# Optimization experiments

Measured on AMD Instinct MI355X. Metric: run time of the kernel, lower is better.

Reference implementation:

```python
import jax, jax.numpy as jnp
import numpy as np

G = 4        # split_group
H = 64       # hidden_size_t = 256 // 4 (causal -> //1)
I = 64       # input_size_t  = 256 // 4
EPS = 1e-5


def _lstm(x, W_ih, W_hh, b):
    """Grouped unidirectional LSTM, PyTorch gate order (i,f,g,o).
    x: (G,B,T,I); W_ih: (G,4H,I); W_hh: (G,4H,H); b: (G,4H) -> (G,B,T,H)"""
    g, bsz, t, _ = x.shape
    h_dim = W_hh.shape[-1]
    # precompute input projections for all timesteps
    xp = jnp.einsum('gbti,gki->gbtk', x, W_ih) + b[:, None, None, :]  # (G,B,T,4H)
    xp = jnp.moveaxis(xp, 2, 0)  # (T,G,B,4H)

    def step(carry, xt):
        h, c = carry
        gates = xt + jnp.einsum('gbh,gkh->gbk', h, W_hh)
        i_g, f_g, g_g, o_g = jnp.split(gates, 4, axis=-1)
        i_g = jax.nn.sigmoid(i_g)
        f_g = jax.nn.sigmoid(f_g)
        g_g = jnp.tanh(g_g)
        o_g = jax.nn.sigmoid(o_g)
        c = f_g * c + i_g * g_g
        h = o_g * jnp.tanh(c)
        return (h, c), h

    h0 = jnp.zeros((g, bsz, h_dim), x.dtype)
    _, hs = jax.lax.scan(step, (h0, h0), xp)  # hs: (T,G,B,H)
    return jnp.moveaxis(hs, 0, 2)  # (G,B,T,H)


def _bn(x, gamma, beta):
    """BatchNorm1d (training stats) over (B,T) per feature. x: (B,T,F)"""
    mean = x.mean(axis=(0, 1))
    var = x.var(axis=(0, 1))
    return (x - mean) * jax.lax.rsqrt(var + EPS) * gamma + beta


def setup_inputs() -> dict:
    key = jax.random.key(0)
    ks = jax.random.split(key, 12)
    s = 0.1
    F = G * H
    return {
        'inpt': jax.random.normal(ks[0], (32, 1000, 256), jnp.float32),
        'W_ih1': jax.random.normal(ks[1], (G, 4 * H, I), jnp.float32) * s,
        'W_hh1': jax.random.normal(ks[2], (G, 4 * H, H), jnp.float32) * s,
        'b1': jax.random.normal(ks[3], (G, 4 * H), jnp.float32) * s,
        'W_ih2': jax.random.normal(ks[4], (G, 4 * H, H), jnp.float32) * s,
        'W_hh2': jax.random.normal(ks[5], (G, 4 * H, H), jnp.float32) * s,
        'b2': jax.random.normal(ks[6], (G, 4 * H), jnp.float32) * s,
        'gamma1': jnp.ones((F,), jnp.float32) + jax.random.normal(ks[7], (F,)) * 0.01,
        'beta1': jax.random.normal(ks[8], (F,), jnp.float32) * 0.01,
        'gamma2': jnp.ones((F,), jnp.float32) + jax.random.normal(ks[9], (F,)) * 0.01,
        'beta2': jax.random.normal(ks[10], (F,), jnp.float32) * 0.01,
    }


def reference(inpt, W_ih1, W_hh1, b1, W_ih2, W_hh2, b2, gamma1, beta1, gamma2, beta2):
    B, T, F = inpt.shape
    # chunk along features -> (G,B,T,I)
    xg = jnp.transpose(inpt.reshape(B, T, G, I), (2, 0, 1, 3))
    y1 = _lstm(xg, W_ih1, W_hh1, b1)  # (G,B,T,H)
    # torch.stack(dim=-1) + flatten: feature index = h*G + g (interleaved)
    x = jnp.transpose(y1, (1, 2, 3, 0)).reshape(B, T, H * G)
    x = _bn(x, gamma1, beta1)
    # chunk again into G contiguous groups of size H
    xg2 = jnp.transpose(x.reshape(B, T, G, H), (2, 0, 1, 3))
    y2 = _lstm(xg2, W_ih2, W_hh2, b2)  # (G,B,T,H)
    # torch.cat(dim=-1): contiguous groups
    x = jnp.transpose(y2, (1, 2, 0, 3)).reshape(B, T, G * H)
    x = _bn(x, gamma2, beta2)
    return x
```

## Files before the change

kernel.cpp:

```cpp
#include <hip/hip_runtime.h>
#include <math.h>

#define G 4
#define H 64
#define T 1000
#define B 32
#define F 256
#define ROWS (B*T)

__device__ __forceinline__ float sigm(float x) {
    return 1.f / (1.f + __expf(-x));
}
__device__ __forceinline__ float tanh_f(float x) {
    return 2.f / (1.f + __expf(-2.f * x)) - 1.f;
}

template<int LAYER>
__global__ __launch_bounds__(256, 1)
void rec_kernel(const float* __restrict__ xin,
                const float* __restrict__ Wih,
                const float* __restrict__ Whh,
                const float* __restrict__ bias,
                const float* __restrict__ bnac,
                float* __restrict__ out)
{
    const int g = blockIdx.x & 3;
    const int b = blockIdx.x >> 2;
    const int k = threadIdx.x;

    __shared__ __align__(16) float xsh[2][64];
    __shared__ __align__(16) float hsh[64];
    __shared__ __align__(16) float gsh[256];

    float wih[64], whh[64];
    {
        const float4* wi = (const float4*)(Wih + (size_t)(g * 256 + k) * 64);
        const float4* wh = (const float4*)(Whh + (size_t)(g * 256 + k) * 64);
        #pragma unroll
        for (int i = 0; i < 16; ++i) {
            float4 v = wi[i];
            wih[4*i] = v.x; wih[4*i+1] = v.y; wih[4*i+2] = v.z; wih[4*i+3] = v.w;
            float4 u = wh[i];
            whh[4*i] = u.x; whh[4*i+1] = u.y; whh[4*i+2] = u.z; whh[4*i+3] = u.w;
        }
    }
    const float bk = bias[g * 256 + k];

    const long rowbase = (long)b * T;
    const int  colbase = g * 64;

    float c = 0.f, af = 1.f, cf = 0.f;
    float xa = 0.f, xb = 0.f;

    if (k < 64) {
        if (LAYER == 2) { af = bnac[colbase + k]; cf = bnac[256 + colbase + k]; }
        hsh[k] = 0.f;
        float x0 = xin[(rowbase + 0) * 256 + colbase + k];
        xsh[0][k] = (LAYER == 2) ? fmaf(x0, af, cf) : x0;
        int t1 = (1 < T) ? 1 : T - 1;
        int t2 = (2 < T) ? 2 : T - 1;
        xa = xin[(rowbase + t1) * 256 + colbase + k];
        xb = xin[(rowbase + t2) * 256 + colbase + k];
    }
    __syncthreads();

    for (int t = 0; t < T; ++t) {
        const int cur = t & 1;

        float xn = 0.f;
        if (k < 64) {
            int tp = t + 3; if (tp > T - 1) tp = T - 1;
            xn = xin[(rowbase + tp) * 256 + colbase + k];
        }

        const float* xs = xsh[cur];
        float a0 = 0.f, a1 = 0.f, a2 = 0.f, a3 = 0.f;
        #pragma unroll
        for (int i = 0; i < 64; i += 4) {
            a0 = fmaf(wih[i],     xs[i],     a0);
            a1 = fmaf(wih[i + 1], xs[i + 1], a1);
            a2 = fmaf(wih[i + 2], xs[i + 2], a2);
            a3 = fmaf(wih[i + 3], xs[i + 3], a3);
        }
        #pragma unroll
        for (int j = 0; j < 64; j += 4) {
            a0 = fmaf(whh[j],     hsh[j],     a0);
            a1 = fmaf(whh[j + 1], hsh[j + 1], a1);
            a2 = fmaf(whh[j + 2], hsh[j + 2], a2);
            a3 = fmaf(whh[j + 3], hsh[j + 3], a3);
        }
        const float acc = bk + ((a0 + a1) + (a2 + a3));

        const float act = (k >= 128 && k < 192) ? tanh_f(acc) : sigm(acc);
        gsh[k] = act;
        __syncthreads();

        if (k < 64) {
            const float ig = gsh[k];
            const float fg = gsh[64 + k];
            const float gg = gsh[128 + k];
            const float og = gsh[192 + k];
            c = fmaf(fg, c, ig * gg);
            const float h = og * tanh_f(c);
            hsh[k] = h;
            const long row = rowbase + t;
            if (LAYER == 1) out[row * 256 + k * 4 + g] = h;
            else            out[row * 256 + colbase + k] = h;
            xsh[cur ^ 1][k] = fmaf(xa, af, cf);
            xa = xb; xb = xn;
        }
        __syncthreads();
    }
}

__global__ void zero_ws(float* sums) {
    int i = blockIdx.x * blockDim.x + threadIdx.x;
    if (i < 512) sums[i] = 0.f;
}

__global__ __launch_bounds__(256) void stats_reduce(const float* __restrict__ x,
                                                    float* __restrict__ sums)
{
    float s = 0.f, ss = 0.f;
    for (int r = blockIdx.x; r < ROWS; r += gridDim.x) {
        float v = x[(long)r * 256 + threadIdx.x];
        s += v;
        ss = fmaf(v, v, ss);
    }
    atomicAdd(&sums[threadIdx.x], s);
    atomicAdd(&sums[256 + threadIdx.x], ss);
}

__global__ void stats_finalize(const float* __restrict__ sums,
                               const float* __restrict__ gamma,
                               const float* __restrict__ beta,
                               float* __restrict__ ac)
{
    int f = threadIdx.x;
    const float invN = 1.f / (float)ROWS;
    float mean = sums[f] * invN;
    float var  = fmaf(-mean, mean, sums[256 + f] * invN);
    float a = gamma[f] * rsqrtf(var + 1e-5f);
    ac[f]       = a;
    ac[256 + f] = fmaf(-mean, a, beta[f]);
}

__global__ __launch_bounds__(256) void bn_apply(float* __restrict__ x,
                                                const float* __restrict__ ac)
{
    __shared__ float a_s[256], c_s[256];
    a_s[threadIdx.x] = ac[threadIdx.x];
    c_s[threadIdx.x] = ac[256 + threadIdx.x];
    __syncthreads();
    const long n4 = (long)ROWS * 64;
    for (long i = (long)blockIdx.x * blockDim.x + threadIdx.x; i < n4;
         i += (long)gridDim.x * blockDim.x) {
        float4 v = ((float4*)x)[i];
        int f0 = (int)((i * 4) & 255);
        v.x = fmaf(v.x, a_s[f0],     c_s[f0]);
        v.y = fmaf(v.y, a_s[f0 + 1], c_s[f0 + 1]);
        v.z = fmaf(v.z, a_s[f0 + 2], c_s[f0 + 2]);
        v.w = fmaf(v.w, a_s[f0 + 3], c_s[f0 + 3]);
        ((float4*)x)[i] = v;
    }
}

extern "C" void kernel_launch(void* const* d_in, const int* in_sizes, int n_in,
                              void* d_out, int out_size, void* d_ws, size_t ws_size,
                              hipStream_t stream)
{
    const float* inpt   = (const float*)d_in[0];
    const float* Wih1   = (const float*)d_in[1];
    const float* Whh1   = (const float*)d_in[2];
    const float* b1     = (const float*)d_in[3];
    const float* Wih2   = (const float*)d_in[4];
    const float* Whh2   = (const float*)d_in[5];
    const float* b2     = (const float*)d_in[6];
    const float* gamma1 = (const float*)d_in[7];
    const float* beta1  = (const float*)d_in[8];
    const float* gamma2 = (const float*)d_in[9];
    const float* beta2  = (const float*)d_in[10];
    float* out  = (float*)d_out;
    float* sums = (float*)d_ws;
    float* ac   = sums + 512;

    zero_ws<<<2, 256, 0, stream>>>(sums);
    rec_kernel<1><<<G * B, 256, 0, stream>>>(inpt, Wih1, Whh1, b1, nullptr, out);

    stats_reduce<<<256, 256, 0, stream>>>(out, sums);
    stats_finalize<<<1, 256, 0, stream>>>(sums, gamma1, beta1, ac);

    rec_kernel<2><<<G * B, 256, 0, stream>>>(out, Wih2, Whh2, b2, ac, out);

    zero_ws<<<2, 256, 0, stream>>>(sums);
    stats_reduce<<<256, 256, 0, stream>>>(out, sums);
    stats_finalize<<<1, 256, 0, stream>>>(sums, gamma2, beta2, ac);
    bn_apply<<<2048, 256, 0, stream>>>(out, ac);
}
```

Measured before the change: 1.680 ms.

## Precompute input projections in parallel GEMM and slim recurrent step loop

Moves the input-to-hidden projection out of the sequential recurrence into a tiled shared-memory GEMM kernel that writes gate pre-activations to workspace, chunked over time when workspace is limited. The recurrent kernel then computes only the hidden-to-hidden product, exchanges gate activations through wavefront shuffles instead of shared memory, and needs one barrier per step instead of two. This shortens the serial critical path at the cost of extra global traffic for the projection buffer and more kernel launches. The old fused path is kept as a fallback when the workspace is too small.

```diff
diff --git a/kernel.cpp b/kernel.cpp
--- a/kernel.cpp
+++ b/kernel.cpp
@@ -5,7 +5,6 @@
 #define H 64
 #define T 1000
 #define B 32
-#define F 256
 #define ROWS (B*T)
 
 __device__ __forceinline__ float sigm(float x) {
@@ -13,6 +12,180 @@
 }
 __device__ __forceinline__ float tanh_f(float x) {
     return 2.f / (1.f + __expf(-2.f * x)) - 1.f;
+}
+
+template<bool BN>
+__global__ __launch_bounds__(256)
+void xp_proj(const float* __restrict__ xin,
+             const float* __restrict__ Wih,
+             const float* __restrict__ bias,
+             const float* __restrict__ ac,
+             float* __restrict__ xp,
+             int t0, int tcn, int tcmax, int TT)
+{
+    int id = blockIdx.x;
+    const int kt = id & 3; id >>= 2;
+    const int tt = id % TT; id /= TT;
+    const int b = id & 31;
+    const int g = id >> 5;
+
+    __shared__ __align__(16) float xs[64][68];
+    __shared__ __align__(16) float ws[64][68];
+
+    const int tx = threadIdx.x & 15, ty = threadIdx.x >> 4;
+
+    #pragma unroll
+    for (int j = 0; j < 4; ++j) {
+        int idx = j * 1024 + threadIdx.x * 4;
+        int r = idx >> 6, ci = idx & 63;
+        float4 v = *(const float4*)&Wih[(size_t)((g * 256 + kt * 64 + r) << 6) + ci];
+        *(float4*)&ws[r][ci] = v;
+    }
+    #pragma unroll
+    for (int j = 0; j < 4; ++j) {
+        int idx = j * 1024 + threadIdx.x * 4;
+        int r = idx >> 6, ci = idx & 63;
+        int tg = t0 + tt * 64 + r; if (tg > T - 1) tg = T - 1;
+        float4 v = *(const float4*)&xin[((size_t)b * T + tg) * 256 + g * 64 + ci];
+        if (BN) {
+            float4 a4 = *(const float4*)&ac[g * 64 + ci];
+            float4 c4 = *(const float4*)&ac[256 + g * 64 + ci];
+            v.x = fmaf(v.x, a4.x, c4.x);
+            v.y = fmaf(v.y, a4.y, c4.y);
+            v.z = fmaf(v.z, a4.z, c4.z);
+            v.w = fmaf(v.w, a4.w, c4.w);
+        }
+        *(float4*)&xs[r][ci] = v;
+    }
+    __syncthreads();
+
+    float acc[4][4] = {};
+    #pragma unroll
+    for (int i4 = 0; i4 < 16; ++i4) {
+        float4 xv[4], wv[4];
+        #pragma unroll
+        for (int q = 0; q < 4; ++q) xv[q] = *(const float4*)&xs[ty * 4 + q][i4 * 4];
+        #pragma unroll
+        for (int q = 0; q < 4; ++q) wv[q] = *(const float4*)&ws[tx * 4 + q][i4 * 4];
+        #pragma unroll
+        for (int a = 0; a < 4; ++a)
+            #pragma unroll
+            for (int c = 0; c < 4; ++c) {
+                acc[a][c] = fmaf(xv[a].x, wv[c].x, acc[a][c]);
+                acc[a][c] = fmaf(xv[a].y, wv[c].y, acc[a][c]);
+                acc[a][c] = fmaf(xv[a].z, wv[c].z, acc[a][c]);
+                acc[a][c] = fmaf(xv[a].w, wv[c].w, acc[a][c]);
+            }
+    }
+
+    const int kbase = kt * 64 + tx * 4;
+    const float4 b4 = *(const float4*)&bias[g * 256 + kbase];
+    float* xpb = xp + (size_t)(g * 32 + b) * tcmax * 256;
+    #pragma unroll
+    for (int a = 0; a < 4; ++a) {
+        int tloc = tt * 64 + ty * 4 + a;
+        if (tloc < tcn) {
+            float4 o;
+            o.x = acc[a][0] + b4.x;
+            o.y = acc[a][1] + b4.y;
+            o.z = acc[a][2] + b4.z;
+            o.w = acc[a][3] + b4.w;
+            *(float4*)&xpb[(size_t)tloc * 256 + kbase] = o;
+        }
+    }
+}
+
+template<int LAYER>
+__global__ __launch_bounds__(256, 1)
+void rec_xp(const float* __restrict__ xp,
+            const float* __restrict__ Whh,
+            float* __restrict__ out,
+            float* __restrict__ stateh, float* __restrict__ statec,
+            int t0, int t1, int tcmax)
+{
+    const int blk = blockIdx.x;
+    const int g = blk & 3, b = blk >> 2;
+    const int l  = threadIdx.x & 63;
+    const int w  = threadIdx.x >> 6;
+    const int gt = l >> 4, c16 = l & 15;
+    const int col = w * 16 + c16;
+    const int row = gt * 64 + col;
+
+    __shared__ __align__(16) float hsh[2][64];
+
+    float whh[64];
+    {
+        const float4* wp = (const float4*)&Whh[(size_t)((g * 256 + row) << 6)];
+        #pragma unroll
+        for (int i = 0; i < 16; ++i) {
+            float4 v = wp[i];
+            whh[4*i] = v.x; whh[4*i+1] = v.y; whh[4*i+2] = v.z; whh[4*i+3] = v.w;
+        }
+    }
+    const float m  = (gt == 2) ? 2.f : 1.f;
+    const float A  = (gt == 2) ? 2.f : 1.f;
+    const float Bc = (gt == 2) ? -1.f : 0.f;
+
+    float cst;
+    if (t0 == 0) {
+        cst = 0.f;
+        if (threadIdx.x < 64) hsh[0][threadIdx.x] = 0.f;
+    } else {
+        cst = statec[blk * 64 + col];
+        if (threadIdx.x < 64) hsh[0][threadIdx.x] = stateh[blk * 64 + threadIdx.x];
+    }
+
+    const float* xpb = xp + (size_t)(g * 32 + b) * tcmax * 256 + row;
+    float p[4];
+    #pragma unroll
+    for (int j = 0; j < 4; ++j) {
+        int tp = t0 + j; if (tp > t1 - 1) tp = t1 - 1;
+        p[j] = xpb[(size_t)(tp - t0) * 256];
+    }
+    __syncthreads();
+
+    float hl = 0.f;
+    const int nsteps = t1 - t0;
+    for (int s = 0; s < nsteps; s += 4) {
+        #pragma unroll
+        for (int j = 0; j < 4; ++j) {
+            const int cur = j & 1;
+            float a0 = 0.f, a1 = 0.f, a2 = 0.f, a3 = 0.f;
+            const float4* hv = (const float4*)hsh[cur];
+            #pragma unroll
+            for (int q = 0; q < 16; ++q) {
+                float4 z = hv[q];
+                a0 = fmaf(whh[4*q],   z.x, a0);
+                a1 = fmaf(whh[4*q+1], z.y, a1);
+                a2 = fmaf(whh[4*q+2], z.z, a2);
+                a3 = fmaf(whh[4*q+3], z.w, a3);
+            }
+            float acc = p[j] + ((a0 + a1) + (a2 + a3));
+            {
+                int tp = t0 + s + j + 4; if (tp > t1 - 1) tp = t1 - 1;
+                p[j] = xpb[(size_t)(tp - t0) * 256];
+            }
+            float act = A / (1.f + __expf(-m * acc)) + Bc;
+            float ig = __shfl(act, c16);
+            float fg = __shfl(act, c16 + 16);
+            float gg = __shfl(act, c16 + 32);
+            float og = __shfl(act, c16 + 48);
+            cst = fmaf(fg, cst, ig * gg);
+            float h = og * tanh_f(cst);
+            if (gt == 0) {
+                hsh[cur ^ 1][col] = h;
+                int t = t0 + s + j;
+                if (LAYER == 1) out[((size_t)b * T + t) * 256 + col * 4 + g] = h;
+                else            out[((size_t)b * T + t) * 256 + g * 64 + col] = h;
+            }
+            hl = h;
+            __syncthreads();
+        }
+    }
+    if (gt == 0) {
+        stateh[blk * 64 + col] = hl;
+        statec[blk * 64 + col] = cst;
+    }
 }
 
 template<int LAYER>
@@ -45,7 +218,6 @@
         }
     }
     const float bk = bias[g * 256 + k];
-
     const long rowbase = (long)b * T;
     const int  colbase = g * 64;
 
@@ -57,22 +229,18 @@
         hsh[k] = 0.f;
         float x0 = xin[(rowbase + 0) * 256 + colbase + k];
         xsh[0][k] = (LAYER == 2) ? fmaf(x0, af, cf) : x0;
-        int t1 = (1 < T) ? 1 : T - 1;
-        int t2 = (2 < T) ? 2 : T - 1;
-        xa = xin[(rowbase + t1) * 256 + colbase + k];
-        xb = xin[(rowbase + t2) * 256 + colbase + k];
+        xa = xin[(rowbase + 1) * 256 + colbase + k];
+        xb = xin[(rowbase + 2) * 256 + colbase + k];
     }
     __syncthreads();
 
     for (int t = 0; t < T; ++t) {
         const int cur = t & 1;
-
         float xn = 0.f;
         if (k < 64) {
             int tp = t + 3; if (tp > T - 1) tp = T - 1;
             xn = xin[(rowbase + tp) * 256 + colbase + k];
         }
-
         const float* xs = xsh[cur];
         float a0 = 0.f, a1 = 0.f, a2 = 0.f, a3 = 0.f;
         #pragma unroll
@@ -83,14 +251,13 @@
             a3 = fmaf(wih[i + 3], xs[i + 3], a3);
         }
         #pragma unroll
-        for (int j = 0; j < 64; j += 4) {
-            a0 = fmaf(whh[j],     hsh[j],     a0);
-            a1 = fmaf(whh[j + 1], hsh[j + 1], a1);
-            a2 = fmaf(whh[j + 2], hsh[j + 2], a2);
-            a3 = fmaf(whh[j + 3], hsh[j + 3], a3);
+        for (int jq = 0; jq < 64; jq += 4) {
+            a0 = fmaf(whh[jq],     hsh[jq],     a0);
+            a1 = fmaf(whh[jq + 1], hsh[jq + 1], a1);
+            a2 = fmaf(whh[jq + 2], hsh[jq + 2], a2);
+            a3 = fmaf(whh[jq + 3], hsh[jq + 3], a3);
         }
         const float acc = bk + ((a0 + a1) + (a2 + a3));
-
         const float act = (k >= 128 && k < 192) ? tanh_f(acc) : sigm(acc);
         gsh[k] = act;
         __syncthreads();
@@ -103,9 +270,9 @@
             c = fmaf(fg, c, ig * gg);
             const float h = og * tanh_f(c);
             hsh[k] = h;
-            const long row = rowbase + t;
-            if (LAYER == 1) out[row * 256 + k * 4 + g] = h;
-            else            out[row * 256 + colbase + k] = h;
+            const long rrow = rowbase + t;
+            if (LAYER == 1) out[rrow * 256 + k * 4 + g] = h;
+            else            out[rrow * 256 + colbase + k] = h;
             xsh[cur ^ 1][k] = fmaf(xa, af, cf);
             xa = xb; xb = xn;
         }
@@ -181,19 +348,49 @@
     const float* gamma2 = (const float*)d_in[9];
     const float* beta2  = (const float*)d_in[10];
     float* out  = (float*)d_out;
+
     float* sums = (float*)d_ws;
-    float* ac   = sums + 512;
-
-    zero_ws<<<2, 256, 0, stream>>>(sums);
-    rec_kernel<1><<<G * B, 256, 0, stream>>>(inpt, Wih1, Whh1, b1, nullptr, out);
-
-    stats_reduce<<<256, 256, 0, stream>>>(out, sums);
-    stats_finalize<<<1, 256, 0, stream>>>(sums, gamma1, beta1, ac);
-
-    rec_kernel<2><<<G * B, 256, 0, stream>>>(out, Wih2, Whh2, b2, ac, out);
-
-    zero_ws<<<2, 256, 0, stream>>>(sums);
-    stats_reduce<<<256, 256, 0, stream>>>(out, sums);
-    stats_finalize<<<1, 256, 0, stream>>>(sums, gamma2, beta2, ac);
-    bn_apply<<<2048, 256, 0, stream>>>(out, ac);
-}
+    float* acbn = sums + 512;
+    float* sth  = acbn + 512;
+    float* stc  = sth + 8192;
+    float* xpb  = stc + 8192;
+
+    const size_t fixedB = (size_t)(512 + 512 + 8192 + 8192) * 4;
+    long availT = ((long)ws_size - (long)fixedB) / (128L * 256L * 4L);
+    int Tcmax = (availT >= T) ? T : (int)(availT & ~3L);
+
+    if (Tcmax >= 100) {
+        zero_ws<<<2, 256, 0, stream>>>(sums);
+        for (int t0 = 0; t0 < T; t0 += Tcmax) {
+            int tcn = T - t0; if (tcn > Tcmax) tcn = Tcmax;
+            int TT = (tcn + 63) / 64;
+            xp_proj<false><<<128 * TT * 4, 256, 0, stream>>>(
+                inpt, Wih1, b1, nullptr, xpb, t0, tcn, Tcmax, TT);
+            rec_xp<1><<<128, 256, 0, stream>>>(xpb, Whh1, out, sth, stc, t0, t0 + tcn, Tcmax);
+        }
+        stats_reduce<<<256, 256, 0, stream>>>(out, sums);
+        stats_finalize<<<1, 256, 0, stream>>>(sums, gamma1, beta1, acbn);
+
+        for (int t0 = 0; t0 < T; t0 += Tcmax) {
+            int tcn = T - t0; if (tcn > Tcmax) tcn = Tcmax;
+            int TT = (tcn + 63) / 64;
+            xp_proj<true><<<128 * TT * 4, 256, 0, stream>>>(
+                out, Wih2, b2, acbn, xpb, t0, tcn, Tcmax, TT);
+            rec_xp<2><<<128, 256, 0, stream>>>(xpb, Whh2, out, sth, stc, t0, t0 + tcn, Tcmax);
+        }
+        zero_ws<<<2, 256, 0, stream>>>(sums);
+        stats_reduce<<<256, 256, 0, stream>>>(out, sums);
+        stats_finalize<<<1, 256, 0, stream>>>(sums, gamma2, beta2, acbn);
+        bn_apply<<<2048, 256, 0, stream>>>(out, acbn);
+    } else {
+        zero_ws<<<2, 256, 0, stream>>>(sums);
+        rec_kernel<1><<<G * B, 256, 0, stream>>>(inpt, Wih1, Whh1, b1, nullptr, out);
+        stats_reduce<<<256, 256, 0, stream>>>(out, sums);
+        stats_finalize<<<1, 256, 0, stream>>>(sums, gamma1, beta1, acbn);
+        rec_kernel<2><<<G * B, 256, 0, stream>>>(out, Wih2, Whh2, b2, acbn, out);
+        zero_ws<<<2, 256, 0, stream>>>(sums);
+        stats_reduce<<<256, 256, 0, stream>>>(out, sums);
+        stats_finalize<<<1, 256, 0, stream>>>(sums, gamma2, beta2, acbn);
+        bn_apply<<<2048, 256, 0, stream>>>(out, acbn);
+    }
+}
```

New measurement: 1.691 ms. No clear change (+0.6%).
